# Performance work log

Measured on AMD Instinct MI355X. Metric: run time of the kernel, lower is better.

Reference implementation:

```python
import jax, jax.numpy as jnp
import numpy as np

B, M, N, C = 8192, 16, 256, 64


def setup_inputs() -> dict:
    key = jax.random.key(0)
    k1, k2 = jax.random.split(key)
    inputs = jax.random.normal(k1, (B, M, C), dtype=jnp.float32)
    codebook = jax.random.normal(k2, (M, N, C), dtype=jnp.float32)
    return {"inputs": inputs, "codebook": codebook}


def reference(inputs, codebook):
    # inputs: [B, M, C]; codebook: [M, N, C]
    # (avoids materializing the torch [B, M, N, C] broadcast difference)
    x2 = jnp.sum(inputs * inputs, axis=-1)[:, :, None]          # [B, M, 1]
    c2 = jnp.sum(codebook * codebook, axis=-1)[None, :, :]      # [1, M, N]
    xc = jnp.einsum('bmc,mnc->bmn', inputs, codebook)           # [B, M, N]
    dist = x2 - 2.0 * xc + c2                                   # [B, M, N]
    idx = jnp.argmin(dist, axis=-1)                             # [B, M] int
    m_idx = jnp.arange(codebook.shape[0])[None, :]              # [1, M]
    codes = codebook[m_idx, idx]                                # [B, M, C]
    return codes, idx
```

## Files before the change

kernel.cpp:

```cpp
#include <hip/hip_runtime.h>
#include <hip/hip_bf16.h>
#include <float.h>


#define BQ 8192
#define MQ 16
#define NQ 256
#define CQ 64

typedef short  shortx8 __attribute__((ext_vector_type(8)));
typedef float  f32x4   __attribute__((ext_vector_type(4)));

#define HI_MASK 0xffff0000u

__device__ __forceinline__ void split3_pair(float a, float b,
                                            uint& q0, uint& q1, uint& q2) {
    const uint ba = __builtin_bit_cast(uint, a);
    const uint bb = __builtin_bit_cast(uint, b);
    q0 = (ba >> 16) | (bb & HI_MASK);
    const float r1a = a - __builtin_bit_cast(float, ba & HI_MASK);
    const float r1b = b - __builtin_bit_cast(float, bb & HI_MASK);
    const uint c1a = __builtin_bit_cast(uint, r1a);
    const uint c1b = __builtin_bit_cast(uint, r1b);
    q1 = (c1a >> 16) | (c1b & HI_MASK);
    const float r2a = r1a - __builtin_bit_cast(float, c1a & HI_MASK);
    const float r2b = r1b - __builtin_bit_cast(float, c1b & HI_MASK);
    q2 = (__builtin_bit_cast(uint, r2a) >> 16) |
         (__builtin_bit_cast(uint, r2b) & HI_MASK);
}

__global__ __launch_bounds__(128) void fq_prep_kernel(
        const float* __restrict__ codebook,
        unsigned short* __restrict__ cb3f,
        float* __restrict__ c2) {
    const int t  = blockIdx.x * 128 + threadIdx.x;
    const int kc = t & 7;
    const int e  = t >> 3;
    const int m  = e >> 8, n = e & 255;
    const int nt = n >> 4, col = n & 15;
    const int h = kc >> 2, quad = kc & 3;

    const float* src = codebook + (size_t)e * CQ + kc * 8;
    const float4 va = *(const float4*)src;
    const float4 vb = *(const float4*)(src + 4);
    const float el[8] = {va.x, va.y, va.z, va.w, vb.x, vb.y, vb.z, vb.w};

    float s = 0.0f;
    #pragma unroll
    for (int u = 0; u < 8; ++u) s = fmaf(el[u], el[u], s);
    s += __shfl_xor(s, 1, 64);
    s += __shfl_xor(s, 2, 64);
    s += __shfl_xor(s, 4, 64);
    if (kc == 0) c2[e] = s;

    uint p0[4], p1[4], p2[4];
    #pragma unroll
    for (int u = 0; u < 4; ++u)
        split3_pair(el[2 * u], el[2 * u + 1], p0[u], p1[u], p2[u]);

    const int lane_f = quad * 16 + col;
    #pragma unroll
    for (int j = 0; j < 3; ++j) {
        const uint* p = (j == 0) ? p0 : (j == 1) ? p1 : p2;
        const int frag = ((m * 3 + j) * 2 + h) * 16 + nt;
        uint4* dst = (uint4*)(cb3f + ((size_t)frag * 64 + lane_f) * 8);
        *dst = make_uint4(p[0], p[1], p[2], p[3]);
    }
}

__global__ __launch_bounds__(256, 4) void fq_main_kernel(
        const float* __restrict__ inputs,
        const float* __restrict__ codebook,
        const unsigned short* __restrict__ cb3f,
        const float* __restrict__ c2,
        float* __restrict__ out_codes,
        float* __restrict__ out_idx) {
    const int m    = blockIdx.y;
    const int row0 = blockIdx.x * 32;
    const int w    = threadIdx.x >> 6;
    const int lane = threadIdx.x & 63;
    const int quad = lane >> 4;
    const int col  = lane & 15;
    const int rg   = w & 1;
    const int chh  = w >> 1;

    __shared__ float sxf[32][68];
    __shared__ float s_c2[NQ];
    __shared__ float s_wb[2][32];
    __shared__ int   s_wi[2][32];
    __shared__ int   s_win[32];

    s_c2[threadIdx.x] = c2[m * NQ + threadIdx.x];

    #pragma unroll
    for (int i = 0; i < 2; ++i) {
        const int f = threadIdx.x + 256 * i;
        const int r = f >> 4;
        const int c = (f & 15) * 4;
        const float4 v = *(const float4*)(
            inputs + ((size_t)(row0 + r) * MQ + m) * CQ + c);
        *(float4*)&sxf[r][c] = v;
    }
    __syncthreads();

    shortx8 bfr[8];
    {
        const int frag0 = (m * 3 * 2) * 16 + chh * 8;
        const unsigned short* bp = cb3f + ((size_t)frag0 * 64 + lane) * 8;
        #pragma unroll
        for (int nt = 0; nt < 8; ++nt)
            bfr[nt] = *(const shortx8*)(bp + (size_t)nt * 64 * 8);
    }

    shortx8 afr[3][2];
    #pragma unroll
    for (int h = 0; h < 2; ++h) {
        const float* xp = &sxf[rg * 16 + col][h * 32 + quad * 8];
        const float4 va = *(const float4*)xp;
        const float4 vb = *(const float4*)(xp + 4);
        const float el[8] = {va.x, va.y, va.z, va.w, vb.x, vb.y, vb.z, vb.w};
        uint q0[4], q1[4], q2[4];
        #pragma unroll
        for (int u = 0; u < 4; ++u)
            split3_pair(el[2 * u], el[2 * u + 1], q0[u], q1[u], q2[u]);
        afr[0][h] = __builtin_bit_cast(shortx8,
            make_uint4(q0[0], q0[1], q0[2], q0[3]));
        afr[1][h] = __builtin_bit_cast(shortx8,
            make_uint4(q1[0], q1[1], q1[2], q1[3]));
        afr[2][h] = __builtin_bit_cast(shortx8,
            make_uint4(q2[0], q2[1], q2[2], q2[3]));
    }

    f32x4 acc[8];
    #pragma unroll
    for (int nt = 0; nt < 8; ++nt)
        acc[nt] = (f32x4){0.f, 0.f, 0.f, 0.f};

    #pragma unroll
    for (int h = 0; h < 2; ++h) {
        #pragma unroll
        for (int j = 0; j < 3; ++j) {
            if (!(h == 0 && j == 0)) {
                const int frag0 = ((m * 3 + j) * 2 + h) * 16 + chh * 8;
                const unsigned short* bp =
                    cb3f + ((size_t)frag0 * 64 + lane) * 8;
                #pragma unroll
                for (int nt = 0; nt < 8; ++nt)
                    bfr[nt] = *(const shortx8*)(bp + (size_t)nt * 64 * 8);
            }
            #pragma unroll
            for (int i = 0; i <= 2 - j; ++i) {
                #pragma unroll
                for (int nt = 0; nt < 8; ++nt)
                    acc[nt] = __builtin_amdgcn_mfma_f32_16x16x32_bf16(
                        afr[i][h], bfr[nt], acc[nt], 0, 0, 0);
            }
        }
    }

    float c2r[8];
    #pragma unroll
    for (int nt = 0; nt < 8; ++nt)
        c2r[nt] = s_c2[chh * 128 + nt * 16 + col];

    #pragma unroll
    for (int reg = 0; reg < 4; ++reg) {
        float bd = FLT_MAX; int bi = 0;
        #pragma unroll
        for (int nt = 0; nt < 8; ++nt) {
            const float d = fmaf(-2.0f, acc[nt][reg], c2r[nt]);
            if (d < bd) { bd = d; bi = chh * 128 + nt * 16 + col; }
        }
        #pragma unroll
        for (int mask = 1; mask <= 8; mask <<= 1) {
            const float od = __shfl_xor(bd, mask, 64);
            const int   oi = __shfl_xor(bi, mask, 64);
            if (od < bd || (od == bd && oi < bi)) { bd = od; bi = oi; }
        }
        if (col == 0) {
            const int r = rg * 16 + quad * 4 + reg;
            s_wb[chh][r] = bd;
            s_wi[chh][r] = bi;
        }
    }
    __syncthreads();

    if (w == 0 && lane < 32) {
        float bd = s_wb[0][lane]; int bi = s_wi[0][lane];
        const float od = s_wb[1][lane]; const int oi = s_wi[1][lane];
        if (od < bd || (od == bd && oi < bi)) { bd = od; bi = oi; }
        s_win[lane] = bi;
        out_idx[(size_t)(row0 + lane) * MQ + m] = (float)bi;
    }
    __syncthreads();

    const float* cbm = codebook + (size_t)m * NQ * CQ;
    #pragma unroll 4
    for (int jj = 0; jj < 8; ++jj) {
        const int r  = w * 8 + jj;
        const int bn = s_win[r];
        out_codes[((size_t)(row0 + r) * MQ + m) * CQ + lane] =
            cbm[(size_t)bn * CQ + lane];
    }
}

extern "C" void kernel_launch(void* const* d_in, const int* in_sizes, int n_in,
                              void* d_out, int out_size, void* d_ws, size_t ws_size,
                              hipStream_t stream) {
    const float* inputs   = (const float*)d_in[0];
    const float* codebook = (const float*)d_in[1];
    float* out_codes = (float*)d_out;
    float* out_idx   = (float*)d_out + (size_t)BQ * MQ * CQ;
    float*          c2   = (float*)d_ws;
    unsigned short* cb3f = (unsigned short*)(c2 + MQ * NQ);

    fq_prep_kernel<<<dim3(256), 128, 0, stream>>>(codebook, cb3f, c2);

    fq_main_kernel<<<dim3(BQ / 32, MQ), 256, 0, stream>>>(
        inputs, codebook, cb3f, c2, out_codes, out_idx);
}
```

Baseline: 122.5 us.

## Fuse codebook prep into main kernel with LDS-resident splits and pipelined input tiles

Removes the separate prep kernel: each block now builds its factor's three-way bf16 codebook split and the squared norms directly in LDS. Each block then loops over 8 tiles of 64 rows. This replaces the per-block re-reading of the full split codebook from global/L2 with reuse from LDS. Input tiles are double-buffered with swizzled async global-to-LDS loads so the next tile's fetch overlaps compute and the gather. The costs are redundant codebook preprocessing across the 16 blocks per factor, a large LDS footprint limiting residency to about one 512-thread block per CU, and only 256 blocks in the grid.

```diff
diff --git a/kernel.cpp b/kernel.cpp
--- a/kernel.cpp
+++ b/kernel.cpp
@@ -7,6 +7,8 @@
 #define MQ 16
 #define NQ 256
 #define CQ 64
+#define RPB 512
+#define NTILES 8
 
 typedef short  shortx8 __attribute__((ext_vector_type(8)));
 typedef float  f32x4   __attribute__((ext_vector_type(4)));
@@ -29,178 +31,179 @@
          (__builtin_bit_cast(uint, r2b) & HI_MASK);
 }
 
-__global__ __launch_bounds__(128) void fq_prep_kernel(
-        const float* __restrict__ codebook,
-        unsigned short* __restrict__ cb3f,
-        float* __restrict__ c2) {
-    const int t  = blockIdx.x * 128 + threadIdx.x;
-    const int kc = t & 7;
-    const int e  = t >> 3;
-    const int m  = e >> 8, n = e & 255;
-    const int nt = n >> 4, col = n & 15;
-    const int h = kc >> 2, quad = kc & 3;
-
-    const float* src = codebook + (size_t)e * CQ + kc * 8;
-    const float4 va = *(const float4*)src;
-    const float4 vb = *(const float4*)(src + 4);
-    const float el[8] = {va.x, va.y, va.z, va.w, vb.x, vb.y, vb.z, vb.w};
-
-    float s = 0.0f;
+__device__ __forceinline__ void fq_stage(const float* __restrict__ inputs,
+        int row0, int m, float* buf, int w, int lane) {
     #pragma unroll
-    for (int u = 0; u < 8; ++u) s = fmaf(el[u], el[u], s);
-    s += __shfl_xor(s, 1, 64);
-    s += __shfl_xor(s, 2, 64);
-    s += __shfl_xor(s, 4, 64);
-    if (kc == 0) c2[e] = s;
-
-    uint p0[4], p1[4], p2[4];
-    #pragma unroll
-    for (int u = 0; u < 4; ++u)
-        split3_pair(el[2 * u], el[2 * u + 1], p0[u], p1[u], p2[u]);
-
-    const int lane_f = quad * 16 + col;
-    #pragma unroll
-    for (int j = 0; j < 3; ++j) {
-        const uint* p = (j == 0) ? p0 : (j == 1) ? p1 : p2;
-        const int frag = ((m * 3 + j) * 2 + h) * 16 + nt;
-        uint4* dst = (uint4*)(cb3f + ((size_t)frag * 64 + lane_f) * 8);
-        *dst = make_uint4(p[0], p[1], p[2], p[3]);
+    for (int i = 0; i < 2; ++i) {
+        const int blk = i * 8 + w;
+        const int f   = (blk << 6) + lane;
+        const int r   = f >> 4;
+        const int c   = (f & 15) ^ (r & 7);
+        const float* src = inputs + ((size_t)(row0 + r) * MQ + m) * CQ + (c << 2);
+        __builtin_amdgcn_global_load_lds(
+            (const __attribute__((address_space(1))) void*)src,
+            (__attribute__((address_space(3))) void*)(buf + (blk << 8)),
+            16, 0, 0);
     }
 }
 
-__global__ __launch_bounds__(256, 4) void fq_main_kernel(
+__global__ __launch_bounds__(512, 2) void fq_fused_kernel(
         const float* __restrict__ inputs,
         const float* __restrict__ codebook,
-        const unsigned short* __restrict__ cb3f,
-        const float* __restrict__ c2,
         float* __restrict__ out_codes,
         float* __restrict__ out_idx) {
     const int m    = blockIdx.y;
-    const int row0 = blockIdx.x * 32;
-    const int w    = threadIdx.x >> 6;
-    const int lane = threadIdx.x & 63;
+    const int rowB = blockIdx.x * RPB;
+    const int w    = (int)threadIdx.x >> 6;
+    const int lane = (int)threadIdx.x & 63;
     const int quad = lane >> 4;
     const int col  = lane & 15;
-    const int rg   = w & 1;
-    const int chh  = w >> 1;
-
-    __shared__ float sxf[32][68];
-    __shared__ float s_c2[NQ];
-    __shared__ float s_wb[2][32];
-    __shared__ int   s_wi[2][32];
-    __shared__ int   s_win[32];
-
-    s_c2[threadIdx.x] = c2[m * NQ + threadIdx.x];
-
+    const int rw   = w & 3;
+    const int chh  = w >> 2;
+
+    __shared__ unsigned short lds_b[96 * 512];
+    __shared__ float sx[2][64][64];
+    __shared__ float s_c2v[NQ];
+    __shared__ float s_wb[2][64];
+    __shared__ int   s_wi[2][64];
+    __shared__ int   s_win[64];
+
+    fq_stage(inputs, rowB,      m, &sx[0][0][0], w, lane);
+    fq_stage(inputs, rowB + 64, m, &sx[1][0][0], w, lane);
+
+    const float* cbm = codebook + (size_t)m * NQ * CQ;
     #pragma unroll
-    for (int i = 0; i < 2; ++i) {
-        const int f = threadIdx.x + 256 * i;
-        const int r = f >> 4;
-        const int c = (f & 15) * 4;
-        const float4 v = *(const float4*)(
-            inputs + ((size_t)(row0 + r) * MQ + m) * CQ + c);
-        *(float4*)&sxf[r][c] = v;
+    for (int it = 0; it < 4; ++it) {
+        const int item = (int)threadIdx.x + it * 512;
+        const int kc = item & 7;
+        const int n  = item >> 3;
+        const int nt = n >> 4, cc = n & 15;
+        const int h = kc >> 2, q = kc & 3;
+        const float* src = cbm + (size_t)n * CQ + kc * 8;
+        const float4 va = *(const float4*)src;
+        const float4 vb = *(const float4*)(src + 4);
+        const float el[8] = {va.x, va.y, va.z, va.w, vb.x, vb.y, vb.z, vb.w};
+
+        float s = 0.0f;
+        #pragma unroll
+        for (int u = 0; u < 8; ++u) s = fmaf(el[u], el[u], s);
+        s += __shfl_xor(s, 1, 64);
+        s += __shfl_xor(s, 2, 64);
+        s += __shfl_xor(s, 4, 64);
+        if (kc == 0) s_c2v[n] = s;
+
+        uint p0[4], p1[4], p2[4];
+        #pragma unroll
+        for (int u = 0; u < 4; ++u)
+            split3_pair(el[2 * u], el[2 * u + 1], p0[u], p1[u], p2[u]);
+        const int lf = q * 16 + cc;
+        #pragma unroll
+        for (int j = 0; j < 3; ++j) {
+            const uint* p = (j == 0) ? p0 : (j == 1) ? p1 : p2;
+            unsigned short* dst =
+                &lds_b[(((j << 1) + h) * 16 + nt) * 512 + lf * 8];
+            *(uint4*)dst = make_uint4(p[0], p[1], p[2], p[3]);
+        }
     }
     __syncthreads();
-
-    shortx8 bfr[8];
-    {
-        const int frag0 = (m * 3 * 2) * 16 + chh * 8;
-        const unsigned short* bp = cb3f + ((size_t)frag0 * 64 + lane) * 8;
-        #pragma unroll
-        for (int nt = 0; nt < 8; ++nt)
-            bfr[nt] = *(const shortx8*)(bp + (size_t)nt * 64 * 8);
-    }
-
-    shortx8 afr[3][2];
-    #pragma unroll
-    for (int h = 0; h < 2; ++h) {
-        const float* xp = &sxf[rg * 16 + col][h * 32 + quad * 8];
-        const float4 va = *(const float4*)xp;
-        const float4 vb = *(const float4*)(xp + 4);
-        const float el[8] = {va.x, va.y, va.z, va.w, vb.x, vb.y, vb.z, vb.w};
-        uint q0[4], q1[4], q2[4];
-        #pragma unroll
-        for (int u = 0; u < 4; ++u)
-            split3_pair(el[2 * u], el[2 * u + 1], q0[u], q1[u], q2[u]);
-        afr[0][h] = __builtin_bit_cast(shortx8,
-            make_uint4(q0[0], q0[1], q0[2], q0[3]));
-        afr[1][h] = __builtin_bit_cast(shortx8,
-            make_uint4(q1[0], q1[1], q1[2], q1[3]));
-        afr[2][h] = __builtin_bit_cast(shortx8,
-            make_uint4(q2[0], q2[1], q2[2], q2[3]));
-    }
-
-    f32x4 acc[8];
-    #pragma unroll
-    for (int nt = 0; nt < 8; ++nt)
-        acc[nt] = (f32x4){0.f, 0.f, 0.f, 0.f};
-
-    #pragma unroll
-    for (int h = 0; h < 2; ++h) {
-        #pragma unroll
-        for (int j = 0; j < 3; ++j) {
-            if (!(h == 0 && j == 0)) {
-                const int frag0 = ((m * 3 + j) * 2 + h) * 16 + chh * 8;
-                const unsigned short* bp =
-                    cb3f + ((size_t)frag0 * 64 + lane) * 8;
-                #pragma unroll
-                for (int nt = 0; nt < 8; ++nt)
-                    bfr[nt] = *(const shortx8*)(bp + (size_t)nt * 64 * 8);
-            }
-            #pragma unroll
-            for (int i = 0; i <= 2 - j; ++i) {
-                #pragma unroll
-                for (int nt = 0; nt < 8; ++nt)
-                    acc[nt] = __builtin_amdgcn_mfma_f32_16x16x32_bf16(
-                        afr[i][h], bfr[nt], acc[nt], 0, 0, 0);
-            }
-        }
-    }
 
     float c2r[8];
     #pragma unroll
     for (int nt = 0; nt < 8; ++nt)
-        c2r[nt] = s_c2[chh * 128 + nt * 16 + col];
-
-    #pragma unroll
-    for (int reg = 0; reg < 4; ++reg) {
-        float bd = FLT_MAX; int bi = 0;
-        #pragma unroll
-        for (int nt = 0; nt < 8; ++nt) {
-            const float d = fmaf(-2.0f, acc[nt][reg], c2r[nt]);
-            if (d < bd) { bd = d; bi = chh * 128 + nt * 16 + col; }
-        }
-        #pragma unroll
-        for (int mask = 1; mask <= 8; mask <<= 1) {
-            const float od = __shfl_xor(bd, mask, 64);
-            const int   oi = __shfl_xor(bi, mask, 64);
+        c2r[nt] = s_c2v[chh * 128 + nt * 16 + col];
+
+    #pragma unroll 1
+    for (int t = 0; t < NTILES; ++t) {
+        const int row0 = rowB + t * 64;
+        const float* sxb = &sx[t & 1][0][0];
+
+        shortx8 afr[3][2];
+        const int r = rw * 16 + col;
+        const float* rowp = sxb + r * 64;
+        #pragma unroll
+        for (int h = 0; h < 2; ++h) {
+            const int p0i = (h * 8 + quad * 2) ^ (r & 7);
+            const float4 va = *(const float4*)(rowp + (p0i << 2));
+            const float4 vb = *(const float4*)(rowp + ((p0i ^ 1) << 2));
+            const float el[8] = {va.x, va.y, va.z, va.w, vb.x, vb.y, vb.z, vb.w};
+            uint q0[4], q1[4], q2[4];
+            #pragma unroll
+            for (int u = 0; u < 4; ++u)
+                split3_pair(el[2 * u], el[2 * u + 1], q0[u], q1[u], q2[u]);
+            afr[0][h] = __builtin_bit_cast(shortx8,
+                make_uint4(q0[0], q0[1], q0[2], q0[3]));
+            afr[1][h] = __builtin_bit_cast(shortx8,
+                make_uint4(q1[0], q1[1], q1[2], q1[3]));
+            afr[2][h] = __builtin_bit_cast(shortx8,
+                make_uint4(q2[0], q2[1], q2[2], q2[3]));
+        }
+
+        f32x4 acc[8];
+        #pragma unroll
+        for (int nt = 0; nt < 8; ++nt)
+            acc[nt] = (f32x4){0.f, 0.f, 0.f, 0.f};
+
+        #pragma unroll
+        for (int h = 0; h < 2; ++h) {
+            #pragma unroll
+            for (int j = 0; j < 3; ++j) {
+                shortx8 bfr[8];
+                #pragma unroll
+                for (int nt = 0; nt < 8; ++nt)
+                    bfr[nt] = *(const shortx8*)
+                        &lds_b[(((j << 1) + h) * 16 + chh * 8 + nt) * 512
+                               + lane * 8];
+                #pragma unroll
+                for (int i = 0; i <= 2 - j; ++i) {
+                    #pragma unroll
+                    for (int nt = 0; nt < 8; ++nt)
+                        acc[nt] = __builtin_amdgcn_mfma_f32_16x16x32_bf16(
+                            afr[i][h], bfr[nt], acc[nt], 0, 0, 0);
+                }
+            }
+        }
+
+        #pragma unroll
+        for (int reg = 0; reg < 4; ++reg) {
+            float bd = FLT_MAX; int bi = 0;
+            #pragma unroll
+            for (int nt = 0; nt < 8; ++nt) {
+                const float d = fmaf(-2.0f, acc[nt][reg], c2r[nt]);
+                if (d < bd) { bd = d; bi = chh * 128 + nt * 16 + col; }
+            }
+            #pragma unroll
+            for (int mask = 1; mask <= 8; mask <<= 1) {
+                const float od = __shfl_xor(bd, mask, 64);
+                const int   oi = __shfl_xor(bi, mask, 64);
+                if (od < bd || (od == bd && oi < bi)) { bd = od; bi = oi; }
+            }
+            if (col == 0) {
+                const int rr = rw * 16 + quad * 4 + reg;
+                s_wb[chh][rr] = bd;
+                s_wi[chh][rr] = bi;
+            }
+        }
+        __syncthreads();
+
+        if (w == 0) {
+            float bd = s_wb[0][lane]; int bi = s_wi[0][lane];
+            const float od = s_wb[1][lane]; const int oi = s_wi[1][lane];
             if (od < bd || (od == bd && oi < bi)) { bd = od; bi = oi; }
-        }
-        if (col == 0) {
-            const int r = rg * 16 + quad * 4 + reg;
-            s_wb[chh][r] = bd;
-            s_wi[chh][r] = bi;
-        }
-    }
-    __syncthreads();
-
-    if (w == 0 && lane < 32) {
-        float bd = s_wb[0][lane]; int bi = s_wi[0][lane];
-        const float od = s_wb[1][lane]; const int oi = s_wi[1][lane];
-        if (od < bd || (od == bd && oi < bi)) { bd = od; bi = oi; }
-        s_win[lane] = bi;
-        out_idx[(size_t)(row0 + lane) * MQ + m] = (float)bi;
-    }
-    __syncthreads();
-
-    const float* cbm = codebook + (size_t)m * NQ * CQ;
-    #pragma unroll 4
-    for (int jj = 0; jj < 8; ++jj) {
-        const int r  = w * 8 + jj;
-        const int bn = s_win[r];
-        out_codes[((size_t)(row0 + r) * MQ + m) * CQ + lane] =
-            cbm[(size_t)bn * CQ + lane];
+            s_win[lane] = bi;
+            out_idx[(size_t)(row0 + lane) * MQ + m] = (float)bi;
+        }
+        __syncthreads();
+
+        if (t + 2 < NTILES)
+            fq_stage(inputs, row0 + 128, m, &sx[t & 1][0][0], w, lane);
+
+        #pragma unroll 4
+        for (int jj = 0; jj < 8; ++jj) {
+            const int rr = w * 8 + jj;
+            const int bn = s_win[rr];
+            out_codes[((size_t)(row0 + rr) * MQ + m) * CQ + lane] =
+                cbm[(size_t)bn * CQ + lane];
+        }
     }
 }
 
@@ -211,11 +214,8 @@
     const float* codebook = (const float*)d_in[1];
     float* out_codes = (float*)d_out;
     float* out_idx   = (float*)d_out + (size_t)BQ * MQ * CQ;
-    float*          c2   = (float*)d_ws;
-    unsigned short* cb3f = (unsigned short*)(c2 + MQ * NQ);
-
-    fq_prep_kernel<<<dim3(256), 128, 0, stream>>>(codebook, cb3f, c2);
-
-    fq_main_kernel<<<dim3(BQ / 32, MQ), 256, 0, stream>>>(
-        inputs, codebook, cb3f, c2, out_codes, out_idx);
-}
+    (void)d_ws; (void)ws_size;
+
+    fq_fused_kernel<<<dim3(BQ / RPB, MQ), 512, 0, stream>>>(
+        inputs, codebook, out_codes, out_idx);
+}
```

New measurement: 116.8 us. 4.7% less time.
